# Kernel tuning notes

Measured on AMD Instinct MI355X. Metric: run time of the kernel, lower is better.

The kernel has to match this reference:

```python
import jax, jax.numpy as jnp
import numpy as np

H = 256          # hidden_size
HH, WW = 4, 4
CONV = HH * WW * H   # 4096, conv_out_size
N = 16           # n_subtasks
S = 32           # subtask_size
B = 256          # batch
T = 128          # timesteps
TOT = N + S + H + S + 1 + 1  # 338, RecurrentState width


def setup_inputs() -> dict:
    key = jax.random.key(0)
    ks = jax.random.split(key, 12)
    w = lambda k, shape: (jax.random.normal(k, shape) * 0.02).astype(jnp.float32)
    obs = jax.random.normal(ks[0], (T, B, CONV), jnp.float32)
    task = jax.random.normal(ks[1], (B, N, S), jnp.float32)
    hx0 = jnp.zeros((B, TOT), jnp.float32).at[:, :N].set(1.0 / N)  # uniform pointer init
    return dict(
        obs=obs, task=task, hx0=hx0,
        W_ih=w(ks[2], (3 * H, H)), W_hh=w(ks[3], (3 * H, H)),
        b_ih=jnp.zeros((3 * H,), jnp.float32), b_hh=jnp.zeros((3 * H,), jnp.float32),
        W_f=w(ks[4], (H, CONV + 2 * S + 1)), b_f=jnp.zeros((H,), jnp.float32),
        W_u=w(ks[5], (1, 2 * H)), b_u=jnp.zeros((1,), jnp.float32),
        W_s=w(ks[6], (3, H)), b_s=jnp.zeros((3,), jnp.float32),
        W_pi=w(ks[7], (N, H + S)), b_pi=jnp.zeros((N,), jnp.float32),
        W_beta=w(ks[8], (2, CONV + S)), b_beta=jnp.zeros((2,), jnp.float32),
    )


def reference(obs, task, hx0, W_ih, W_hh, b_ih, b_hh, W_f, b_f, W_u, b_u,
              W_s, b_s, W_pi, b_pi, W_beta, b_beta):
    M = task  # [B, N, S] subtask memory
    p0 = hx0[:, :N]
    r0 = hx0[:, N:N + S]
    h0 = hx0[:, N + S:N + S + H]
    g0 = hx0[:, N + S + H:N + S + H + S]
    b0 = hx0[:, N + S + H + S:N + S + H + S + 1]
    keys = jax.random.split(jax.random.key(42), T * 2).reshape(T, 2)

    def gru(x, h):  # torch.nn.GRUCell math
        gi = x @ W_ih.T + b_ih
        gh = h @ W_hh.T + b_hh
        ir, iz, inn = jnp.split(gi, 3, axis=-1)
        hr, hz, hn = jnp.split(gh, 3, axis=-1)
        rr = jax.nn.sigmoid(ir + hr)
        z = jax.nn.sigmoid(iz + hz)
        n = jnp.tanh(inn + rr * hn)
        return (1.0 - z) * n + z * h

    def step(carry, xs):
        p, r, h, b = carry[0], carry[1], carry[2], carry[4]
        g = carry[3]
        x, kk = xs
        # s = f(cat(x, r, g, b))
        s = jnp.concatenate([x, r, g, b], axis=-1) @ W_f.T + b_f
        # update gate c = sigmoid(phi_update(cat(s, h)))
        c = jax.nn.sigmoid(jnp.concatenate([s, h], axis=-1) @ W_u.T + b_u)  # [B,1]
        h_new = gru(s, h)
        # pointer shift: l = softmax(phi_shift(h_old)); p = conv1d(p, l) (same-pad, k=3)
        l = jax.nn.softmax(h @ W_s.T + b_s, axis=1)  # [B,3]
        pp = jnp.pad(p, ((0, 0), (1, 1)))
        p_new = l[:, 0:1] * pp[:, :N] + l[:, 1:2] * pp[:, 1:N + 1] + l[:, 2:3] * pp[:, 2:N + 2]
        # memory read r = p @ M
        r_new = jnp.einsum('bn,bns->bs', p_new, M)
        p = c * p_new + (1.0 - c) * p
        r = c * r_new + (1.0 - c) * r
        h = c * h_new + (1.0 - c) * h
        # sample g ~ Cat(pi_theta(h, r)); g embedding = selected memory row
        logits_g = jnp.concatenate([h, r], axis=-1) @ W_pi.T + b_pi  # [B,N]
        g_idx = jax.random.categorical(kk[0], logits_g)  # [B] int
        lp_g = jnp.take_along_axis(jax.nn.log_softmax(logits_g, axis=-1), g_idx[:, None], axis=1)  # [B,1]
        g_vec = jnp.take_along_axis(M, g_idx[:, None, None], axis=1)[:, 0, :]  # [B,S]
        g = c * g_vec + (1.0 - c) * g
        # sample b ~ Cat(beta(x, g))
        logits_b = jnp.concatenate([x, g], axis=-1) @ W_beta.T + b_beta  # [B,2]
        b_idx = jax.random.categorical(kk[1], logits_b)
        lp_b = jnp.take_along_axis(jax.nn.log_softmax(logits_b, axis=-1), b_idx[:, None], axis=1)
        b = b_idx[:, None].astype(jnp.float32)
        log_prob = lp_g + lp_b
        out = jnp.concatenate([p, r, h, g, b, log_prob], axis=-1)  # [B, TOT]
        return (p, r, h, g, b), out

    _, outs = jax.lax.scan(step, (p0, r0, h0, g0, b0), (obs, keys))
    return outs  # [T, B, TOT]
```

## Files before the change

kernel.cpp:

```cpp
#include <hip/hip_runtime.h>


#define RNG_PARTITIONABLE 1

#define T_STEPS 128
#define B_ROWS  256
#define TOT     338
#define CONV    4096
#define LDWF    4161
#define LDWB    4128

typedef float v2f __attribute__((ext_vector_type(2)));

__device__ __forceinline__ void tf2x32(unsigned k0, unsigned k1, unsigned c0, unsigned c1,
                                       unsigned &o0, unsigned &o1) {
  const unsigned ks2 = k0 ^ k1 ^ 0x1BD11BDAu;
  unsigned x0 = c0 + k0;
  unsigned x1 = c1 + k1;
#define TFR(r) { x0 += x1; x1 = (x1 << (r)) | (x1 >> (32 - (r))); x1 ^= x0; }
  TFR(13) TFR(15) TFR(26) TFR(6)
  x0 += k1; x1 += ks2 + 1u;
  TFR(17) TFR(29) TFR(16) TFR(24)
  x0 += ks2; x1 += k0 + 2u;
  TFR(13) TFR(15) TFR(26) TFR(6)
  x0 += k0; x1 += k1 + 3u;
  TFR(17) TFR(29) TFR(16) TFR(24)
  x0 += k1; x1 += ks2 + 4u;
  TFR(13) TFR(15) TFR(26) TFR(6)
  x0 += ks2; x1 += k0 + 5u;
#undef TFR
  o0 = x0; o1 = x1;
}

__device__ __forceinline__ void rng_key(unsigned j, unsigned &k0, unsigned &k1) {
#if RNG_PARTITIONABLE
  tf2x32(0u, 42u, 0u, j, k0, k1);
#else
  unsigned w[2];
  for (int q = 0; q < 2; ++q) {
    unsigned i = 2u*j + (unsigned)q, a, b;
    if (i < 256u) { tf2x32(0u, 42u, i, 256u + i, a, b); w[q] = a; }
    else          { tf2x32(0u, 42u, i - 256u, i, a, b); w[q] = b; }
  }
  k0 = w[0]; k1 = w[1];
#endif
}

__device__ __forceinline__ unsigned rng_bits(unsigned k0, unsigned k1, unsigned idx, unsigned total) {
#if RNG_PARTITIONABLE
  unsigned o0, o1;
  tf2x32(k0, k1, 0u, idx, o0, o1);
  return o0 ^ o1;
#else
  unsigned half = total >> 1, o0, o1;
  if (idx < half) { tf2x32(k0, k1, idx, half + idx, o0, o1); return o0; }
  else            { tf2x32(k0, k1, idx - half, idx, o0, o1); return o1; }
#endif
}

__device__ __forceinline__ float gumbel_from_bits(unsigned bits) {
  float u0 = __uint_as_float(0x3f800000u | (bits >> 9)) - 1.0f;
  float u  = fmaxf(u0, 1.17549435e-38f);
  return -logf(-logf(u));
}

__global__ __launch_bounds__(256) void rng_k(float* __restrict__ ggum, float* __restrict__ bgum) {
  unsigned tid = blockIdx.x * 256u + threadIdx.x;
  const unsigned NG = T_STEPS * B_ROWS * 16;
  const unsigned NB = T_STEPS * B_ROWS * 2;
  if (tid < NG) {
    unsigned t = tid / (B_ROWS * 16);
    unsigned i = tid % (B_ROWS * 16);
    unsigned k0, k1; rng_key(2u * t, k0, k1);
    ggum[tid] = gumbel_from_bits(rng_bits(k0, k1, i, B_ROWS * 16));
  } else if (tid < NG + NB) {
    unsigned q = tid - NG;
    unsigned t = q / (B_ROWS * 2);
    unsigned i = q % (B_ROWS * 2);
    unsigned k0, k1; rng_key(2u * t + 1u, k0, k1);
    bgum[q] = gumbel_from_bits(rng_bits(k0, k1, i, B_ROWS * 2));
  }
}

__global__ __launch_bounds__(768) void prep4_k(const float* __restrict__ W_ih,
                                               const float* __restrict__ W_hh,
                                               float4* __restrict__ WT4) {
  int k2 = blockIdx.x;
  int col = threadIdx.x;
  float a0 = W_ih[(size_t)col * 256 + 2 * k2];
  float a1 = W_ih[(size_t)col * 256 + 2 * k2 + 1];
  float b0 = W_hh[(size_t)col * 256 + 2 * k2];
  float b1 = W_hh[(size_t)col * 256 + 2 * k2 + 1];
  WT4[(size_t)k2 * 768 + col] = make_float4(a0, b0, a1, b1);
}

__device__ __forceinline__ float waveRed(float v) {
  v += __shfl_down(v, 32, 64);
  v += __shfl_down(v, 16, 64);
  v += __shfl_down(v, 8, 64);
  v += __shfl_down(v, 4, 64);
  v += __shfl_down(v, 2, 64);
  v += __shfl_down(v, 1, 64);
  return v;
}

__global__ __launch_bounds__(256) void bx_k(const float* __restrict__ obs,
                                            const float* __restrict__ W_beta,
                                            const float* __restrict__ b_beta,
                                            float* __restrict__ bxv) {
  int m = blockIdx.x, tid = threadIdx.x;
  const float* row = obs + (size_t)m * CONV;
  float p0 = 0.f, p1 = 0.f;
  for (int i = tid; i < CONV; i += 256) {
    float o = row[i];
    p0 = fmaf(o, W_beta[i], p0);
    p1 = fmaf(o, W_beta[LDWB + i], p1);
  }
  p0 = waveRed(p0); p1 = waveRed(p1);
  __shared__ float sc[2][4];
  int w = tid >> 6;
  if ((tid & 63) == 0) { sc[0][w] = p0; sc[1][w] = p1; }
  __syncthreads();
  if (tid == 0) bxv[(size_t)m * 2 + 0] = sc[0][0] + sc[0][1] + sc[0][2] + sc[0][3] + b_beta[0];
  if (tid == 1) bxv[(size_t)m * 2 + 1] = sc[1][0] + sc[1][1] + sc[1][2] + sc[1][3] + b_beta[1];
}

struct __attribute__((packed, aligned(4))) F4 { float x, y, z, w; };

__global__ __launch_bounds__(256) void gemm1_k(const float* __restrict__ A,
                                               const float* __restrict__ W,
                                               const float* __restrict__ bias,
                                               float* __restrict__ C1) {
  __shared__ __align__(16) float As[32][68];
  __shared__ __align__(16) float Bs[32][68];
  int bid = blockIdx.x;
  int mt = bid & 511, nt = bid >> 9;
  int m0 = mt * 64, n0 = nt * 64;
  int tid = threadIdx.x;
  int tm = tid & 15, tn = tid >> 4;
  int lr = tid >> 2;
  int lc = (tid & 3) * 8;
  v2f acc[4][2];
#pragma unroll
  for (int i = 0; i < 4; ++i) { acc[i][0] = (v2f){0.f, 0.f}; acc[i][1] = (v2f){0.f, 0.f}; }
  for (int k0 = 0; k0 < CONV; k0 += 32) {
    F4 a0 = *(const F4*)(A + (size_t)(m0 + lr) * CONV + k0 + lc);
    F4 a1 = *(const F4*)(A + (size_t)(m0 + lr) * CONV + k0 + lc + 4);
    F4 b0 = *(const F4*)(W + (size_t)(n0 + lr) * LDWF + k0 + lc);
    F4 b1 = *(const F4*)(W + (size_t)(n0 + lr) * LDWF + k0 + lc + 4);
    __syncthreads();
    As[lc + 0][lr] = a0.x; As[lc + 1][lr] = a0.y; As[lc + 2][lr] = a0.z; As[lc + 3][lr] = a0.w;
    As[lc + 4][lr] = a1.x; As[lc + 5][lr] = a1.y; As[lc + 6][lr] = a1.z; As[lc + 7][lr] = a1.w;
    Bs[lc + 0][lr] = b0.x; Bs[lc + 1][lr] = b0.y; Bs[lc + 2][lr] = b0.z; Bs[lc + 3][lr] = b0.w;
    Bs[lc + 4][lr] = b1.x; Bs[lc + 5][lr] = b1.y; Bs[lc + 6][lr] = b1.z; Bs[lc + 7][lr] = b1.w;
    __syncthreads();
#pragma unroll
    for (int kk = 0; kk < 32; ++kk) {
      const float4 av = *(const float4*)&As[kk][tm * 4];
      const float4 bv = *(const float4*)&Bs[kk][tn * 4];
      const v2f bl = (v2f){bv.x, bv.y};
      const v2f bh = (v2f){bv.z, bv.w};
      const float aa[4] = {av.x, av.y, av.z, av.w};
#pragma unroll
      for (int i = 0; i < 4; ++i) {
        v2f ax = (v2f){aa[i], aa[i]};
        acc[i][0] = __builtin_elementwise_fma(ax, bl, acc[i][0]);
        acc[i][1] = __builtin_elementwise_fma(ax, bh, acc[i][1]);
      }
    }
  }
  const int mrow = m0 + tm * 4;
  const int ncol = n0 + tn * 4;
  float4 bv4 = *(const float4*)(bias + ncol);
#pragma unroll
  for (int i = 0; i < 4; ++i) {
    float4 v;
    v.x = acc[i][0].x + bv4.x; v.y = acc[i][0].y + bv4.y;
    v.z = acc[i][1].x + bv4.z; v.w = acc[i][1].y + bv4.w;
    *(float4*)(C1 + (size_t)(mrow + i) * 256 + ncol) = v;
  }
}

__global__ __launch_bounds__(256, 1) void seq_k(
    const float* __restrict__ hx0, const float* __restrict__ task,
    const float* __restrict__ W_f, const float* __restrict__ WT4,
    const float* __restrict__ b_ih, const float* __restrict__ b_hh,
    const float* __restrict__ W_u, const float* __restrict__ b_u,
    const float* __restrict__ W_s, const float* __restrict__ b_s,
    const float* __restrict__ W_pi, const float* __restrict__ b_pi,
    const float* __restrict__ W_beta, const float* __restrict__ C1,
    const float* __restrict__ bxv, const float* __restrict__ ggum,
    const float* __restrict__ bgum, float* __restrict__ out) {
  const int b2 = blockIdx.x;
  const int tid = threadIdx.x;
  const int o = tid;
  const int brow0 = 2 * b2, brow1 = 2 * b2 + 1;
  const float4* __restrict__ wt = (const float4*)WT4;

  __shared__ float wf_sh[65 * 256];
  __shared__ float wpi_sh[288 * 16];
  __shared__ __align__(16) float4 sh4[2][128];
  __shared__ float M_sh[2][512];
  __shared__ float red4[2][4][4];
  __shared__ float red16[2][4][16];
  __shared__ float p_sh[2][2][16];
  __shared__ float r_sh[2][2][32];
  __shared__ float g_sh[2][2][32];
  __shared__ float gg_sh[2][16], bg_sh[2][2], bx_sh[2][2];
  __shared__ float wb_sh[2][32], bpi_sh[16];

  for (int i = tid; i < 65 * 256; i += 256) {
    int oo = i / 65, j = i % 65;
    wf_sh[i] = W_f[(size_t)oo * LDWF + CONV + j];
  }
  for (int i = tid; i < 288 * 16; i += 256) wpi_sh[i] = W_pi[i];
  float hold0 = hx0[brow0 * TOT + 48 + o];
  float hold1 = hx0[brow1 * TOT + 48 + o];
  ((float*)&sh4[0][o >> 1])[(o & 1) * 2 + 1] = hold0;
  ((float*)&sh4[1][o >> 1])[(o & 1) * 2 + 1] = hold1;
  if (tid < 16) {
    p_sh[0][0][tid] = hx0[brow0 * TOT + tid];
    p_sh[1][0][tid] = hx0[brow1 * TOT + tid];
  }
  if (tid < 32) {
    r_sh[0][0][tid] = hx0[brow0 * TOT + 16 + tid];
    r_sh[1][0][tid] = hx0[brow1 * TOT + 16 + tid];
    g_sh[0][0][tid] = hx0[brow0 * TOT + 304 + tid];
    g_sh[1][0][tid] = hx0[brow1 * TOT + 304 + tid];
    wb_sh[0][tid] = W_beta[CONV + tid];
    wb_sh[1][tid] = W_beta[LDWB + CONV + tid];
  }
  if (tid >= 32 && tid < 48) bpi_sh[tid - 32] = b_pi[tid - 32];
  M_sh[0][tid] = task[(size_t)brow0 * 512 + tid];
  M_sh[0][256 + tid] = task[(size_t)brow0 * 512 + 256 + tid];
  M_sh[1][tid] = task[(size_t)brow1 * 512 + tid];
  M_sh[1][256 + tid] = task[(size_t)brow1 * 512 + 256 + tid];
  float bnew0 = hx0[brow0 * TOT + 336];
  float bnew1 = hx0[brow1 * TOT + 336];

  const float bih_r = b_ih[o], bih_z = b_ih[256 + o], bih_n = b_ih[512 + o];
  const float bhh_r = b_hh[o], bhh_z = b_hh[256 + o], bhh_n = b_hh[512 + o];
  const float wu_s = W_u[o], wu_h = W_u[256 + o];
  const float ws0 = W_s[o], ws1 = W_s[256 + o], ws2 = W_s[512 + o];
  const float bu0 = b_u[0], bs0 = b_s[0], bs1 = b_s[1], bs2 = b_s[2];
  __syncthreads();

  float sacc0, sacc1;
  {
    const float* wfr = wf_sh + o * 65;
    sacc0 = C1[(size_t)brow0 * 256 + o];
    sacc1 = C1[(size_t)brow1 * 256 + o];
#pragma unroll
    for (int j = 0; j < 32; ++j) sacc0 = fmaf(r_sh[0][0][j], wfr[j], sacc0);
#pragma unroll
    for (int j = 0; j < 32; ++j) sacc0 = fmaf(g_sh[0][0][j], wfr[32 + j], sacc0);
    sacc0 = fmaf(bnew0, wfr[64], sacc0);
#pragma unroll
    for (int j = 0; j < 32; ++j) sacc1 = fmaf(r_sh[1][0][j], wfr[j], sacc1);
#pragma unroll
    for (int j = 0; j < 32; ++j) sacc1 = fmaf(g_sh[1][0][j], wfr[32 + j], sacc1);
    sacc1 = fmaf(bnew1, wfr[64], sacc1);
    ((float*)&sh4[0][o >> 1])[(o & 1) * 2] = sacc0;
    ((float*)&sh4[1][o >> 1])[(o & 1) * 2] = sacc1;
  }
  __syncthreads();

  for (int t = 0; t < T_STEPS; ++t) {
    const int pp = t & 1, np = pp ^ 1;

    int tn2 = (t + 1 < T_STEPS) ? t + 1 : t;
    float c1n0 = C1[((size_t)tn2 * 256 + brow0) * 256 + o];
    float c1n1 = C1[((size_t)tn2 * 256 + brow1) * 256 + o];
    if (tid < 32) {
      int rr = tid >> 4, j = tid & 15;
      gg_sh[rr][j] = ggum[((size_t)t * 256 + brow0 + rr) * 16 + j];
    } else if (tid < 36) {
      int q = tid - 32;
      bg_sh[q >> 1][q & 1] = bgum[((size_t)t * 256 + brow0 + (q >> 1)) * 2 + (q & 1)];
    } else if (tid < 40) {
      int q = tid - 36;
      bx_sh[q >> 1][q & 1] = bxv[((size_t)t * 256 + brow0 + (q >> 1)) * 2 + (q & 1)];
    }

    v2f ar0 = (v2f){0.f, 0.f}, az0 = (v2f){0.f, 0.f}, an0 = (v2f){0.f, 0.f};
    v2f ar1 = (v2f){0.f, 0.f}, az1 = (v2f){0.f, 0.f}, an1 = (v2f){0.f, 0.f};
#pragma unroll 4
    for (int k2 = 0; k2 < 128; ++k2) {
      float4 wr = wt[(size_t)(k2 * 3 + 0) * 256 + o];
      float4 wz = wt[(size_t)(k2 * 3 + 1) * 256 + o];
      float4 wn = wt[(size_t)(k2 * 3 + 2) * 256 + o];
      float4 x0 = sh4[0][k2];
      float4 x1 = sh4[1][k2];
      v2f xa0 = (v2f){x0.x, x0.y}, xb0 = (v2f){x0.z, x0.w};
      v2f xa1 = (v2f){x1.x, x1.y}, xb1 = (v2f){x1.z, x1.w};
      ar0 = __builtin_elementwise_fma(xa0, (v2f){wr.x, wr.y}, ar0);
      ar0 = __builtin_elementwise_fma(xb0, (v2f){wr.z, wr.w}, ar0);
      az0 = __builtin_elementwise_fma(xa0, (v2f){wz.x, wz.y}, az0);
      az0 = __builtin_elementwise_fma(xb0, (v2f){wz.z, wz.w}, az0);
      an0 = __builtin_elementwise_fma(xa0, (v2f){wn.x, wn.y}, an0);
      an0 = __builtin_elementwise_fma(xb0, (v2f){wn.z, wn.w}, an0);
      ar1 = __builtin_elementwise_fma(xa1, (v2f){wr.x, wr.y}, ar1);
      ar1 = __builtin_elementwise_fma(xb1, (v2f){wr.z, wr.w}, ar1);
      az1 = __builtin_elementwise_fma(xa1, (v2f){wz.x, wz.y}, az1);
      az1 = __builtin_elementwise_fma(xb1, (v2f){wz.z, wz.w}, az1);
      an1 = __builtin_elementwise_fma(xa1, (v2f){wn.x, wn.y}, an1);
      an1 = __builtin_elementwise_fma(xb1, (v2f){wn.z, wn.w}, an1);
    }
    {
      float pc0 = fmaf(wu_s, sacc0, wu_h * hold0);
      float q00 = ws0 * hold0, q01 = ws1 * hold0, q02 = ws2 * hold0;
      float pc1 = fmaf(wu_s, sacc1, wu_h * hold1);
      float q10 = ws0 * hold1, q11 = ws1 * hold1, q12 = ws2 * hold1;
      pc0 = waveRed(pc0); q00 = waveRed(q00); q01 = waveRed(q01); q02 = waveRed(q02);
      pc1 = waveRed(pc1); q10 = waveRed(q10); q11 = waveRed(q11); q12 = waveRed(q12);
      int w4 = tid >> 6;
      if ((tid & 63) == 0) {
        red4[0][w4][0] = pc0; red4[0][w4][1] = q00; red4[0][w4][2] = q01; red4[0][w4][3] = q02;
        red4[1][w4][0] = pc1; red4[1][w4][1] = q10; red4[1][w4][2] = q11; red4[1][w4][3] = q12;
      }
    }
    __syncthreads();

    float c0, c1, l00, l01, l02, l10, l11, l12;
    {
      float cs0 = red4[0][0][0] + red4[0][1][0] + red4[0][2][0] + red4[0][3][0] + bu0;
      c0 = 1.0f / (1.0f + expf(-cs0));
      float x0 = red4[0][0][1] + red4[0][1][1] + red4[0][2][1] + red4[0][3][1] + bs0;
      float x1 = red4[0][0][2] + red4[0][1][2] + red4[0][2][2] + red4[0][3][2] + bs1;
      float x2 = red4[0][0][3] + red4[0][1][3] + red4[0][2][3] + red4[0][3][3] + bs2;
      float m = fmaxf(x0, fmaxf(x1, x2));
      float e0 = expf(x0 - m), e1 = expf(x1 - m), e2 = expf(x2 - m);
      float es = e0 + e1 + e2;
      l00 = e0 / es; l01 = e1 / es; l02 = e2 / es;
      float cs1 = red4[1][0][0] + red4[1][1][0] + red4[1][2][0] + red4[1][3][0] + bu0;
      c1 = 1.0f / (1.0f + expf(-cs1));
      float y0 = red4[1][0][1] + red4[1][1][1] + red4[1][2][1] + red4[1][3][1] + bs0;
      float y1 = red4[1][0][2] + red4[1][1][2] + red4[1][2][2] + red4[1][3][2] + bs1;
      float y2 = red4[1][0][3] + red4[1][1][3] + red4[1][2][3] + red4[1][3][3] + bs2;
      float mm = fmaxf(y0, fmaxf(y1, y2));
      float f0 = expf(y0 - mm), f1 = expf(y1 - mm), f2 = expf(y2 - mm);
      float fs = f0 + f1 + f2;
      l10 = f0 / fs; l11 = f1 / fs; l12 = f2 / fs;
    }
    const float omc0 = 1.0f - c0, omc1 = 1.0f - c1;
    float pn0[16], pn1[16];
#pragma unroll
    for (int i = 0; i < 16; ++i) {
      float pm0 = (i > 0) ? p_sh[0][pp][i - 1] : 0.f;
      float pq0 = (i < 15) ? p_sh[0][pp][i + 1] : 0.f;
      pn0[i] = l00 * pm0 + l01 * p_sh[0][pp][i] + l02 * pq0;
      float pm1 = (i > 0) ? p_sh[1][pp][i - 1] : 0.f;
      float pq1 = (i < 15) ? p_sh[1][pp][i + 1] : 0.f;
      pn1[i] = l10 * pm1 + l11 * p_sh[1][pp][i] + l12 * pq1;
    }
    float hg0, hg1;
    {
      float rr_ = 1.0f / (1.0f + expf(-(ar0.x + bih_r + ar0.y + bhh_r)));
      float zz = 1.0f / (1.0f + expf(-(az0.x + bih_z + az0.y + bhh_z)));
      float nn = tanhf(an0.x + bih_n + rr_ * (an0.y + bhh_n));
      float hnew = (1.0f - zz) * nn + zz * hold0;
      hg0 = c0 * hnew + omc0 * hold0;
      ((float*)&sh4[0][o >> 1])[(o & 1) * 2 + 1] = hg0;
      float rr1 = 1.0f / (1.0f + expf(-(ar1.x + bih_r + ar1.y + bhh_r)));
      float zz1 = 1.0f / (1.0f + expf(-(az1.x + bih_z + az1.y + bhh_z)));
      float nn1 = tanhf(an1.x + bih_n + rr1 * (an1.y + bhh_n));
      float hnew1 = (1.0f - zz1) * nn1 + zz1 * hold1;
      hg1 = c1 * hnew1 + omc1 * hold1;
      ((float*)&sh4[1][o >> 1])[(o & 1) * 2 + 1] = hg1;
    }
    float rv0 = 0.f, rv1 = 0.f;
    if (tid < 32) {
      float a0 = 0.f, a1 = 0.f;
#pragma unroll
      for (int n2 = 0; n2 < 16; ++n2) a0 = fmaf(pn0[n2], M_sh[0][n2 * 32 + o], a0);
#pragma unroll
      for (int n2 = 0; n2 < 16; ++n2) a1 = fmaf(pn1[n2], M_sh[1][n2 * 32 + o], a1);
      rv0 = c0 * a0 + omc0 * r_sh[0][pp][o];
      rv1 = c1 * a1 + omc1 * r_sh[1][pp][o];
      r_sh[0][np][o] = rv0;
      r_sh[1][np][o] = rv1;
    }
    if (tid < 16) {
      p_sh[0][np][o] = c0 * pn0[o] + omc0 * p_sh[0][pp][o];
      p_sh[1][np][o] = c1 * pn1[o] + omc1 * p_sh[1][pp][o];
    }
    hold0 = hg0; hold1 = hg1;
    __syncthreads();

    {
      float pv0[16], pv1[16];
#pragma unroll
      for (int o2 = 0; o2 < 16; ++o2) {
        pv0[o2] = hg0 * wpi_sh[o2 * 288 + o];
        pv1[o2] = hg1 * wpi_sh[o2 * 288 + o];
      }
      if (tid < 32) {
#pragma unroll
        for (int o2 = 0; o2 < 16; ++o2) {
          pv0[o2] = fmaf(rv0, wpi_sh[o2 * 288 + 256 + o], pv0[o2]);
          pv1[o2] = fmaf(rv1, wpi_sh[o2 * 288 + 256 + o], pv1[o2]);
        }
      }
#pragma unroll
      for (int o2 = 0; o2 < 16; ++o2) { pv0[o2] = waveRed(pv0[o2]); pv1[o2] = waveRed(pv1[o2]); }
      int w4 = tid >> 6;
      if ((tid & 63) == 0) {
#pragma unroll
        for (int o2 = 0; o2 < 16; ++o2) { red16[0][w4][o2] = pv0[o2]; red16[1][w4][o2] = pv1[o2]; }
      }
    }
    __syncthreads();

    int gidx0 = 0, gidx1 = 0;
    float lpg0, lpg1;
    {
      float best = -3.402823466e+38f;
      float lg[16];
#pragma unroll
      for (int n2 = 0; n2 < 16; ++n2)
        lg[n2] = red16[0][0][n2] + red16[0][1][n2] + red16[0][2][n2] + red16[0][3][n2] + bpi_sh[n2];
      for (int n2 = 0; n2 < 16; ++n2) {
        float v = lg[n2] + gg_sh[0][n2];
        if (v > best) { best = v; gidx0 = n2; }
      }
      float mx = lg[0];
      for (int n2 = 1; n2 < 16; ++n2) mx = fmaxf(mx, lg[n2]);
      float se = 0.f;
      for (int n2 = 0; n2 < 16; ++n2) se += expf(lg[n2] - mx);
      lpg0 = lg[gidx0] - mx - logf(se);
      float best1 = -3.402823466e+38f;
#pragma unroll
      for (int n2 = 0; n2 < 16; ++n2)
        lg[n2] = red16[1][0][n2] + red16[1][1][n2] + red16[1][2][n2] + red16[1][3][n2] + bpi_sh[n2];
      for (int n2 = 0; n2 < 16; ++n2) {
        float v = lg[n2] + gg_sh[1][n2];
        if (v > best1) { best1 = v; gidx1 = n2; }
      }
      float mx1 = lg[0];
      for (int n2 = 1; n2 < 16; ++n2) mx1 = fmaxf(mx1, lg[n2]);
      float se1 = 0.f;
      for (int n2 = 0; n2 < 16; ++n2) se1 += expf(lg[n2] - mx1);
      lpg1 = lg[gidx1] - mx1 - logf(se1);
    }
    if (tid < 32) {
      g_sh[0][np][o] = c0 * M_sh[0][gidx0 * 32 + o] + omc0 * g_sh[0][pp][o];
      g_sh[1][np][o] = c1 * M_sh[1][gidx1 * 32 + o] + omc1 * g_sh[1][pp][o];
    }
    __syncthreads();

    float lpt0, lpt1;
    {
      float lb0 = bx_sh[0][0], lb1 = bx_sh[0][1];
      for (int s2 = 0; s2 < 32; ++s2) {
        float gv = g_sh[0][np][s2];
        lb0 = fmaf(gv, wb_sh[0][s2], lb0);
        lb1 = fmaf(gv, wb_sh[1][s2], lb1);
      }
      int bidx = ((lb1 + bg_sh[0][1]) > (lb0 + bg_sh[0][0])) ? 1 : 0;
      float mb = fmaxf(lb0, lb1);
      float seb = expf(lb0 - mb) + expf(lb1 - mb);
      bnew0 = (float)bidx;
      lpt0 = lpg0 + ((bidx ? lb1 : lb0) - mb - logf(seb));
      float mb1_0 = bx_sh[1][0], mb1_1 = bx_sh[1][1];
      for (int s2 = 0; s2 < 32; ++s2) {
        float gv = g_sh[1][np][s2];
        mb1_0 = fmaf(gv, wb_sh[0][s2], mb1_0);
        mb1_1 = fmaf(gv, wb_sh[1][s2], mb1_1);
      }
      int bidx1 = ((mb1_1 + bg_sh[1][1]) > (mb1_0 + bg_sh[1][0])) ? 1 : 0;
      float mbm = fmaxf(mb1_0, mb1_1);
      float seb1 = expf(mb1_0 - mbm) + expf(mb1_1 - mbm);
      bnew1 = (float)bidx1;
      lpt1 = lpg1 + ((bidx1 ? mb1_1 : mb1_0) - mbm - logf(seb1));
    }
    {
      const float* wfr = wf_sh + o * 65;
      sacc0 = c1n0;
#pragma unroll
      for (int j = 0; j < 32; ++j) sacc0 = fmaf(r_sh[0][np][j], wfr[j], sacc0);
#pragma unroll
      for (int j = 0; j < 32; ++j) sacc0 = fmaf(g_sh[0][np][j], wfr[32 + j], sacc0);
      sacc0 = fmaf(bnew0, wfr[64], sacc0);
      ((float*)&sh4[0][o >> 1])[(o & 1) * 2] = sacc0;
      sacc1 = c1n1;
#pragma unroll
      for (int j = 0; j < 32; ++j) sacc1 = fmaf(r_sh[1][np][j], wfr[j], sacc1);
#pragma unroll
      for (int j = 0; j < 32; ++j) sacc1 = fmaf(g_sh[1][np][j], wfr[32 + j], sacc1);
      sacc1 = fmaf(bnew1, wfr[64], sacc1);
      ((float*)&sh4[1][o >> 1])[(o & 1) * 2] = sacc1;
    }
    for (int j = tid; j < TOT; j += 256) {
      float v;
      if (j < 16) v = p_sh[0][np][j];
      else if (j < 48) v = r_sh[0][np][j - 16];
      else if (j < 304) { int hh = j - 48; v = ((const float*)&sh4[0][hh >> 1])[(hh & 1) * 2 + 1]; }
      else if (j < 336) v = g_sh[0][np][j - 304];
      else if (j == 336) v = bnew0;
      else v = lpt0;
      out[((size_t)t * 256 + brow0) * TOT + j] = v;
    }
    for (int j = tid; j < TOT; j += 256) {
      float v;
      if (j < 16) v = p_sh[1][np][j];
      else if (j < 48) v = r_sh[1][np][j - 16];
      else if (j < 304) { int hh = j - 48; v = ((const float*)&sh4[1][hh >> 1])[(hh & 1) * 2 + 1]; }
      else if (j < 336) v = g_sh[1][np][j - 304];
      else if (j == 336) v = bnew1;
      else v = lpt1;
      out[((size_t)t * 256 + brow1) * TOT + j] = v;
    }
    __syncthreads();
  }
}

extern "C" void kernel_launch(void* const* d_in, const int* in_sizes, int n_in,
                              void* d_out, int out_size, void* d_ws, size_t ws_size,
                              hipStream_t stream) {
  const float* obs    = (const float*)d_in[0];
  const float* task   = (const float*)d_in[1];
  const float* hx0    = (const float*)d_in[2];
  const float* W_ih   = (const float*)d_in[3];
  const float* W_hh   = (const float*)d_in[4];
  const float* b_ih   = (const float*)d_in[5];
  const float* b_hh   = (const float*)d_in[6];
  const float* W_f    = (const float*)d_in[7];
  const float* b_f    = (const float*)d_in[8];
  const float* W_u    = (const float*)d_in[9];
  const float* b_u    = (const float*)d_in[10];
  const float* W_s    = (const float*)d_in[11];
  const float* b_s    = (const float*)d_in[12];
  const float* W_pi   = (const float*)d_in[13];
  const float* b_pi   = (const float*)d_in[14];
  const float* W_beta = (const float*)d_in[15];
  const float* b_beta = (const float*)d_in[16];

  char* ws = (char*)d_ws;
  size_t off = 0;
  auto take = [&](size_t bytes) {
    size_t r = off;
    off += (bytes + 255) & ~(size_t)255;
    return r;
  };
  size_t off_WT4  = take((size_t)768 * 256 * 8);
  size_t off_ggum = take((size_t)T_STEPS * B_ROWS * 16 * 4);
  size_t off_bgum = take((size_t)T_STEPS * B_ROWS * 2 * 4);
  size_t off_bx   = take((size_t)T_STEPS * B_ROWS * 2 * 4);
  size_t off_C1   = take((size_t)T_STEPS * B_ROWS * 256 * 4);
  if (off > ws_size) return;

  float* WT4  = (float*)(ws + off_WT4);
  float* ggum = (float*)(ws + off_ggum);
  float* bgum = (float*)(ws + off_bgum);
  float* bxv  = (float*)(ws + off_bx);
  float* C1   = (float*)(ws + off_C1);

  hipLaunchKernelGGL(prep4_k, dim3(128), dim3(768), 0, stream, W_ih, W_hh, (float4*)WT4);
  hipLaunchKernelGGL(rng_k, dim3(2304), dim3(256), 0, stream, ggum, bgum);
  hipLaunchKernelGGL(gemm1_k, dim3(2048), dim3(256), 0, stream, obs, W_f, b_f, C1);
  hipLaunchKernelGGL(bx_k, dim3(32768), dim3(256), 0, stream, obs, W_beta, b_beta, bxv);
  hipLaunchKernelGGL(seq_k, dim3(128), dim3(256), 0, stream,
                     hx0, task, W_f, WT4, b_ih, b_hh, W_u, b_u, W_s, b_s, W_pi, b_pi,
                     W_beta, C1, bxv, ggum, bgum, (float*)d_out);
}
```

Measured before the change: 3.999 ms.

## Double-buffer GRU input, cut per-step barriers, duplicate transposed weights

The per-step shared GRU input buffer is now double-buffered. The update/switch gate reductions for the next step move to the end of the current step, and the new g vector is recomputed inline instead of being read back after a barrier. Together these remove three __syncthreads per timestep. Output writes become direct per-thread stores instead of branchy loops. The transposed GRU weights are duplicated into two copies, with groups of blocks reading different copies, meant to spread L2/channel contention. The cost is extra redundant arithmetic for the g recomputation and twice the weight workspace.

```diff
diff --git a/kernel.cpp b/kernel.cpp
--- a/kernel.cpp
+++ b/kernel.cpp
@@ -85,13 +85,14 @@
 __global__ __launch_bounds__(768) void prep4_k(const float* __restrict__ W_ih,
                                                const float* __restrict__ W_hh,
                                                float4* __restrict__ WT4) {
-  int k2 = blockIdx.x;
+  int k2 = blockIdx.x & 127;
+  int copy = blockIdx.x >> 7;
   int col = threadIdx.x;
   float a0 = W_ih[(size_t)col * 256 + 2 * k2];
   float a1 = W_ih[(size_t)col * 256 + 2 * k2 + 1];
   float b0 = W_hh[(size_t)col * 256 + 2 * k2];
   float b1 = W_hh[(size_t)col * 256 + 2 * k2 + 1];
-  WT4[(size_t)k2 * 768 + col] = make_float4(a0, b0, a1, b1);
+  WT4[(size_t)copy * 98304 + (size_t)k2 * 768 + col] = make_float4(a0, b0, a1, b1);
 }
 
 __device__ __forceinline__ float waveRed(float v) {
@@ -195,11 +196,11 @@
   const int tid = threadIdx.x;
   const int o = tid;
   const int brow0 = 2 * b2, brow1 = 2 * b2 + 1;
-  const float4* __restrict__ wt = (const float4*)WT4;
+  const float4* __restrict__ wt = (const float4*)WT4 + (size_t)((b2 >> 3) & 1) * 98304;
 
   __shared__ float wf_sh[65 * 256];
   __shared__ float wpi_sh[288 * 16];
-  __shared__ __align__(16) float4 sh4[2][128];
+  __shared__ __align__(16) float4 SH4[2][2][128];
   __shared__ float M_sh[2][512];
   __shared__ float red4[2][4][4];
   __shared__ float red16[2][4][16];
@@ -216,8 +217,6 @@
   for (int i = tid; i < 288 * 16; i += 256) wpi_sh[i] = W_pi[i];
   float hold0 = hx0[brow0 * TOT + 48 + o];
   float hold1 = hx0[brow1 * TOT + 48 + o];
-  ((float*)&sh4[0][o >> 1])[(o & 1) * 2 + 1] = hold0;
-  ((float*)&sh4[1][o >> 1])[(o & 1) * 2 + 1] = hold1;
   if (tid < 16) {
     p_sh[0][0][tid] = hx0[brow0 * TOT + tid];
     p_sh[1][0][tid] = hx0[brow1 * TOT + tid];
@@ -260,8 +259,23 @@
 #pragma unroll
     for (int j = 0; j < 32; ++j) sacc1 = fmaf(g_sh[1][0][j], wfr[32 + j], sacc1);
     sacc1 = fmaf(bnew1, wfr[64], sacc1);
-    ((float*)&sh4[0][o >> 1])[(o & 1) * 2] = sacc0;
-    ((float*)&sh4[1][o >> 1])[(o & 1) * 2] = sacc1;
+    ((float*)&SH4[0][0][o >> 1])[(o & 1) * 2]     = sacc0;
+    ((float*)&SH4[0][0][o >> 1])[(o & 1) * 2 + 1] = hold0;
+    ((float*)&SH4[0][1][o >> 1])[(o & 1) * 2]     = sacc1;
+    ((float*)&SH4[0][1][o >> 1])[(o & 1) * 2 + 1] = hold1;
+  }
+  {
+    float pc0 = fmaf(wu_s, sacc0, wu_h * hold0);
+    float q00 = ws0 * hold0, q01 = ws1 * hold0, q02 = ws2 * hold0;
+    float pc1 = fmaf(wu_s, sacc1, wu_h * hold1);
+    float q10 = ws0 * hold1, q11 = ws1 * hold1, q12 = ws2 * hold1;
+    pc0 = waveRed(pc0); q00 = waveRed(q00); q01 = waveRed(q01); q02 = waveRed(q02);
+    pc1 = waveRed(pc1); q10 = waveRed(q10); q11 = waveRed(q11); q12 = waveRed(q12);
+    int w4 = tid >> 6;
+    if ((tid & 63) == 0) {
+      red4[0][w4][0] = pc0; red4[0][w4][1] = q00; red4[0][w4][2] = q01; red4[0][w4][3] = q02;
+      red4[1][w4][0] = pc1; red4[1][w4][1] = q10; red4[1][w4][2] = q11; red4[1][w4][3] = q12;
+    }
   }
   __syncthreads();
 
@@ -289,8 +303,8 @@
       float4 wr = wt[(size_t)(k2 * 3 + 0) * 256 + o];
       float4 wz = wt[(size_t)(k2 * 3 + 1) * 256 + o];
       float4 wn = wt[(size_t)(k2 * 3 + 2) * 256 + o];
-      float4 x0 = sh4[0][k2];
-      float4 x1 = sh4[1][k2];
+      float4 x0 = SH4[pp][0][k2];
+      float4 x1 = SH4[pp][1][k2];
       v2f xa0 = (v2f){x0.x, x0.y}, xb0 = (v2f){x0.z, x0.w};
       v2f xa1 = (v2f){x1.x, x1.y}, xb1 = (v2f){x1.z, x1.w};
       ar0 = __builtin_elementwise_fma(xa0, (v2f){wr.x, wr.y}, ar0);
@@ -306,20 +320,6 @@
       an1 = __builtin_elementwise_fma(xa1, (v2f){wn.x, wn.y}, an1);
       an1 = __builtin_elementwise_fma(xb1, (v2f){wn.z, wn.w}, an1);
     }
-    {
-      float pc0 = fmaf(wu_s, sacc0, wu_h * hold0);
-      float q00 = ws0 * hold0, q01 = ws1 * hold0, q02 = ws2 * hold0;
-      float pc1 = fmaf(wu_s, sacc1, wu_h * hold1);
-      float q10 = ws0 * hold1, q11 = ws1 * hold1, q12 = ws2 * hold1;
-      pc0 = waveRed(pc0); q00 = waveRed(q00); q01 = waveRed(q01); q02 = waveRed(q02);
-      pc1 = waveRed(pc1); q10 = waveRed(q10); q11 = waveRed(q11); q12 = waveRed(q12);
-      int w4 = tid >> 6;
-      if ((tid & 63) == 0) {
-        red4[0][w4][0] = pc0; red4[0][w4][1] = q00; red4[0][w4][2] = q01; red4[0][w4][3] = q02;
-        red4[1][w4][0] = pc1; red4[1][w4][1] = q10; red4[1][w4][2] = q11; red4[1][w4][3] = q12;
-      }
-    }
-    __syncthreads();
 
     float c0, c1, l00, l01, l02, l10, l11, l12;
     {
@@ -343,6 +343,7 @@
       l10 = f0 / fs; l11 = f1 / fs; l12 = f2 / fs;
     }
     const float omc0 = 1.0f - c0, omc1 = 1.0f - c1;
+
     float pn0[16], pn1[16];
 #pragma unroll
     for (int i = 0; i < 16; ++i) {
@@ -360,13 +361,13 @@
       float nn = tanhf(an0.x + bih_n + rr_ * (an0.y + bhh_n));
       float hnew = (1.0f - zz) * nn + zz * hold0;
       hg0 = c0 * hnew + omc0 * hold0;
-      ((float*)&sh4[0][o >> 1])[(o & 1) * 2 + 1] = hg0;
+      ((float*)&SH4[np][0][o >> 1])[(o & 1) * 2 + 1] = hg0;
       float rr1 = 1.0f / (1.0f + expf(-(ar1.x + bih_r + ar1.y + bhh_r)));
       float zz1 = 1.0f / (1.0f + expf(-(az1.x + bih_z + az1.y + bhh_z)));
       float nn1 = tanhf(an1.x + bih_n + rr1 * (an1.y + bhh_n));
       float hnew1 = (1.0f - zz1) * nn1 + zz1 * hold1;
       hg1 = c1 * hnew1 + omc1 * hold1;
-      ((float*)&sh4[1][o >> 1])[(o & 1) * 2 + 1] = hg1;
+      ((float*)&SH4[np][1][o >> 1])[(o & 1) * 2 + 1] = hg1;
     }
     float rv0 = 0.f, rv1 = 0.f;
     if (tid < 32) {
@@ -384,9 +385,6 @@
       p_sh[0][np][o] = c0 * pn0[o] + omc0 * p_sh[0][pp][o];
       p_sh[1][np][o] = c1 * pn1[o] + omc1 * p_sh[1][pp][o];
     }
-    hold0 = hg0; hold1 = hg1;
-    __syncthreads();
-
     {
       float pv0[16], pv1[16];
 #pragma unroll
@@ -409,16 +407,17 @@
         for (int o2 = 0; o2 < 16; ++o2) { red16[0][w4][o2] = pv0[o2]; red16[1][w4][o2] = pv1[o2]; }
       }
     }
+    hold0 = hg0; hold1 = hg1;
     __syncthreads();
 
     int gidx0 = 0, gidx1 = 0;
     float lpg0, lpg1;
     {
-      float best = -3.402823466e+38f;
       float lg[16];
 #pragma unroll
       for (int n2 = 0; n2 < 16; ++n2)
         lg[n2] = red16[0][0][n2] + red16[0][1][n2] + red16[0][2][n2] + red16[0][3][n2] + bpi_sh[n2];
+      float best = -3.402823466e+38f;
       for (int n2 = 0; n2 < 16; ++n2) {
         float v = lg[n2] + gg_sh[0][n2];
         if (v > best) { best = v; gidx0 = n2; }
@@ -446,13 +445,11 @@
       g_sh[0][np][o] = c0 * M_sh[0][gidx0 * 32 + o] + omc0 * g_sh[0][pp][o];
       g_sh[1][np][o] = c1 * M_sh[1][gidx1 * 32 + o] + omc1 * g_sh[1][pp][o];
     }
-    __syncthreads();
-
     float lpt0, lpt1;
     {
       float lb0 = bx_sh[0][0], lb1 = bx_sh[0][1];
       for (int s2 = 0; s2 < 32; ++s2) {
-        float gv = g_sh[0][np][s2];
+        float gv = c0 * M_sh[0][gidx0 * 32 + s2] + omc0 * g_sh[0][pp][s2];
         lb0 = fmaf(gv, wb_sh[0][s2], lb0);
         lb1 = fmaf(gv, wb_sh[1][s2], lb1);
       }
@@ -463,7 +460,7 @@
       lpt0 = lpg0 + ((bidx ? lb1 : lb0) - mb - logf(seb));
       float mb1_0 = bx_sh[1][0], mb1_1 = bx_sh[1][1];
       for (int s2 = 0; s2 < 32; ++s2) {
-        float gv = g_sh[1][np][s2];
+        float gv = c1 * M_sh[1][gidx1 * 32 + s2] + omc1 * g_sh[1][pp][s2];
         mb1_0 = fmaf(gv, wb_sh[0][s2], mb1_0);
         mb1_1 = fmaf(gv, wb_sh[1][s2], mb1_1);
       }
@@ -479,36 +476,53 @@
 #pragma unroll
       for (int j = 0; j < 32; ++j) sacc0 = fmaf(r_sh[0][np][j], wfr[j], sacc0);
 #pragma unroll
-      for (int j = 0; j < 32; ++j) sacc0 = fmaf(g_sh[0][np][j], wfr[32 + j], sacc0);
+      for (int j = 0; j < 32; ++j) {
+        float gv = c0 * M_sh[0][gidx0 * 32 + j] + omc0 * g_sh[0][pp][j];
+        sacc0 = fmaf(gv, wfr[32 + j], sacc0);
+      }
       sacc0 = fmaf(bnew0, wfr[64], sacc0);
-      ((float*)&sh4[0][o >> 1])[(o & 1) * 2] = sacc0;
+      ((float*)&SH4[np][0][o >> 1])[(o & 1) * 2] = sacc0;
       sacc1 = c1n1;
 #pragma unroll
       for (int j = 0; j < 32; ++j) sacc1 = fmaf(r_sh[1][np][j], wfr[j], sacc1);
 #pragma unroll
-      for (int j = 0; j < 32; ++j) sacc1 = fmaf(g_sh[1][np][j], wfr[32 + j], sacc1);
+      for (int j = 0; j < 32; ++j) {
+        float gv = c1 * M_sh[1][gidx1 * 32 + j] + omc1 * g_sh[1][pp][j];
+        sacc1 = fmaf(gv, wfr[32 + j], sacc1);
+      }
       sacc1 = fmaf(bnew1, wfr[64], sacc1);
-      ((float*)&sh4[1][o >> 1])[(o & 1) * 2] = sacc1;
-    }
-    for (int j = tid; j < TOT; j += 256) {
-      float v;
-      if (j < 16) v = p_sh[0][np][j];
-      else if (j < 48) v = r_sh[0][np][j - 16];
-      else if (j < 304) { int hh = j - 48; v = ((const float*)&sh4[0][hh >> 1])[(hh & 1) * 2 + 1]; }
-      else if (j < 336) v = g_sh[0][np][j - 304];
-      else if (j == 336) v = bnew0;
-      else v = lpt0;
-      out[((size_t)t * 256 + brow0) * TOT + j] = v;
-    }
-    for (int j = tid; j < TOT; j += 256) {
-      float v;
-      if (j < 16) v = p_sh[1][np][j];
-      else if (j < 48) v = r_sh[1][np][j - 16];
-      else if (j < 304) { int hh = j - 48; v = ((const float*)&sh4[1][hh >> 1])[(hh & 1) * 2 + 1]; }
-      else if (j < 336) v = g_sh[1][np][j - 304];
-      else if (j == 336) v = bnew1;
-      else v = lpt1;
-      out[((size_t)t * 256 + brow1) * TOT + j] = v;
+      ((float*)&SH4[np][1][o >> 1])[(o & 1) * 2] = sacc1;
+    }
+    {
+      float pc0 = fmaf(wu_s, sacc0, wu_h * hold0);
+      float q00 = ws0 * hold0, q01 = ws1 * hold0, q02 = ws2 * hold0;
+      float pc1 = fmaf(wu_s, sacc1, wu_h * hold1);
+      float q10 = ws0 * hold1, q11 = ws1 * hold1, q12 = ws2 * hold1;
+      pc0 = waveRed(pc0); q00 = waveRed(q00); q01 = waveRed(q01); q02 = waveRed(q02);
+      pc1 = waveRed(pc1); q10 = waveRed(q10); q11 = waveRed(q11); q12 = waveRed(q12);
+      int w4 = tid >> 6;
+      if ((tid & 63) == 0) {
+        red4[0][w4][0] = pc0; red4[0][w4][1] = q00; red4[0][w4][2] = q01; red4[0][w4][3] = q02;
+        red4[1][w4][0] = pc1; red4[1][w4][1] = q10; red4[1][w4][2] = q11; red4[1][w4][3] = q12;
+      }
+    }
+    {
+      size_t base0 = ((size_t)t * 256 + brow0) * TOT;
+      size_t base1 = ((size_t)t * 256 + brow1) * TOT;
+      out[base0 + 48 + o] = hg0;
+      out[base1 + 48 + o] = hg1;
+      if (tid < 16) {
+        out[base0 + tid] = p_sh[0][np][tid];
+        out[base1 + tid] = p_sh[1][np][tid];
+      }
+      if (tid < 32) {
+        out[base0 + 16 + tid] = r_sh[0][np][tid];
+        out[base1 + 16 + tid] = r_sh[1][np][tid];
+        out[base0 + 304 + tid] = c0 * M_sh[0][gidx0 * 32 + tid] + omc0 * g_sh[0][pp][tid];
+        out[base1 + 304 + tid] = c1 * M_sh[1][gidx1 * 32 + tid] + omc1 * g_sh[1][pp][tid];
+      }
+      if (tid == 32) { out[base0 + 336] = bnew0; out[base1 + 336] = bnew1; }
+      if (tid == 33) { out[base0 + 337] = lpt0; out[base1 + 337] = lpt1; }
     }
     __syncthreads();
   }
@@ -542,7 +556,7 @@
     off += (bytes + 255) & ~(size_t)255;
     return r;
   };
-  size_t off_WT4  = take((size_t)768 * 256 * 8);
+  size_t off_WT4  = take((size_t)2 * 98304 * 16);
   size_t off_ggum = take((size_t)T_STEPS * B_ROWS * 16 * 4);
   size_t off_bgum = take((size_t)T_STEPS * B_ROWS * 2 * 4);
   size_t off_bx   = take((size_t)T_STEPS * B_ROWS * 2 * 4);
@@ -555,7 +569,7 @@
   float* bxv  = (float*)(ws + off_bx);
   float* C1   = (float*)(ws + off_C1);
 
-  hipLaunchKernelGGL(prep4_k, dim3(128), dim3(768), 0, stream, W_ih, W_hh, (float4*)WT4);
+  hipLaunchKernelGGL(prep4_k, dim3(256), dim3(768), 0, stream, W_ih, W_hh, (float4*)WT4);
   hipLaunchKernelGGL(rng_k, dim3(2304), dim3(256), 0, stream, ggum, bgum);
   hipLaunchKernelGGL(gemm1_k, dim3(2048), dim3(256), 0, stream, obs, W_f, b_f, C1);
   hipLaunchKernelGGL(bx_k, dim3(32768), dim3(256), 0, stream, obs, W_beta, b_beta, bxv);
```

New measurement: 3.998 ms. About the same (-0.0%).
